# Optimization experiments

Hardware: AMD Instinct MI355X
Metric: run time of the kernel (lower is better)

Reference implementation:

```python
import jax, jax.numpy as jnp
import numpy as np

B, N, Q, D = 1, 6, 10000, 256
HEADS, LEVELS, NPTS, ZANCH = 8, 1, 8, 4  # NPTS = 2*n_points, ZANCH = num_points_in_pillar
HF, WF = 32, 88
HD = D // HEADS


def setup_inputs() -> dict:
    key = jax.random.key(0)
    ks = jax.random.split(key, 18)
    s = 1.0 / np.sqrt(D)
    inp = {
        'queries': jax.random.normal(ks[0], (B, N, Q, D), jnp.float32),
        'pos_emb': jax.random.normal(ks[1], (B, N, Q, D), jnp.float32),
        'lvl_emb': jax.random.normal(ks[2], (LEVELS, D), jnp.float32),
        'cam_emb': jax.random.normal(ks[3], (N, D), jnp.float32),
        'features0': jax.random.normal(ks[4], (B * N, D, HF, WF), jnp.float32),
        'reference_points_3D': jax.random.uniform(ks[5], (B, N, Q, ZANCH, 2), jnp.float32),
        'bev_mask': jax.random.randint(ks[6], (B, N, Q, ZANCH, 2), 0, 2).astype(bool),
        # MSDeformAttn3D params
        'W_value': jax.random.normal(ks[7], (D, D), jnp.float32) * s,
        'b_value': jnp.zeros((D,), jnp.float32),
        'W_off': jax.random.normal(ks[8], (HEADS * LEVELS * NPTS * 2, D), jnp.float32) * 0.01,
        'b_off': jax.random.uniform(ks[9], (HEADS * LEVELS * NPTS * 2,), jnp.float32, -2.0, 2.0),
        'W_attn': jax.random.normal(ks[10], (HEADS * LEVELS * NPTS, D), jnp.float32) * s,
        'b_attn': jnp.zeros((HEADS * LEVELS * NPTS,), jnp.float32),
        'W_inner': jax.random.normal(ks[11], (D, D), jnp.float32) * s,
        'b_inner': jnp.zeros((D,), jnp.float32),
        # SpatialCrossAttention.output_proj
        'W_out': jax.random.normal(ks[12], (D, D), jnp.float32) * s,
        'b_out': jnp.zeros((D,), jnp.float32),
    }
    return inp


def _bilinear(value_t, loc, H, W):
    # value_t: (bn, heads, H*W, hd); loc: (bn, q, heads, pts, 2) normalized to [0,1]
    bn, q, heads, pts, _ = loc.shape
    hd = value_t.shape[-1]
    # grid_sample(2*loc-1, align_corners=False) -> pixel coord = loc*size - 0.5
    x = loc[..., 0] * W - 0.5
    y = loc[..., 1] * H - 0.5
    x0 = jnp.floor(x); y0 = jnp.floor(y)
    dx = x - x0; dy = y - y0
    x0 = x0.astype(jnp.int32); y0 = y0.astype(jnp.int32)
    out = jnp.zeros((bn, heads, q * pts, hd), value_t.dtype)
    corners = ((0, 0, (1 - dx) * (1 - dy)), (1, 0, dx * (1 - dy)),
               (0, 1, (1 - dx) * dy), (1, 1, dx * dy))
    for ox, oy, w in corners:
        xi = x0 + ox; yi = y0 + oy
        valid = (xi >= 0) & (xi < W) & (yi >= 0) & (yi < H)  # zero padding
        wgt = jnp.where(valid, w, 0.0)
        idx = jnp.clip(yi, 0, H - 1) * W + jnp.clip(xi, 0, W - 1)  # (bn,q,heads,pts)
        idx_t = idx.transpose(0, 2, 1, 3).reshape(bn, heads, q * pts)
        g = jnp.take_along_axis(value_t, idx_t[..., None], axis=2)  # (bn,heads,q*pts,hd)
        wgt_t = wgt.transpose(0, 2, 1, 3).reshape(bn, heads, q * pts)
        out = out + g * wgt_t[..., None]
    return out.reshape(bn, heads, q, pts, hd)


def _forward(queries, pos_emb, lvl_emb, cam_emb, features0, reference_points_3D, bev_mask,
             W_value, b_value, W_off, b_off, W_attn, b_attn, W_inner, b_inner, W_out, b_out):
    b, n, q, d = queries.shape
    hf, wf = features0.shape[-2:]
    # flatten features + level/cam embeddings -> (b*n, hw, d)
    feat = features0.reshape(b, n, d, hf * wf)
    feat = feat + lvl_emb[0][None, None, :, None] + cam_emb[None, :, :, None]
    input_flatten = feat.transpose(0, 1, 3, 2).reshape(b * n, hf * wf, d)

    qp = (queries + pos_emb).reshape(b * n, q, d)
    ref = reference_points_3D.reshape(b * n, q, ZANCH, 2)

    # --- MSDeformAttn3D (single level) ---
    value = (input_flatten @ W_value.T + b_value).reshape(b * n, hf * wf, HEADS, HD)
    off = (qp @ W_off.T + b_off).reshape(b * n, q, HEADS, LEVELS, NPTS, 2)
    attw = jax.nn.softmax((qp @ W_attn.T + b_attn).reshape(b * n, q, HEADS, LEVELS * NPTS), axis=-1)
    attw = attw.reshape(b * n, q, HEADS, LEVELS, NPTS)
    normalizer = jnp.array([wf, hf], queries.dtype)  # (W, H)
    pts_per_z = NPTS // ZANCH
    off_z = off.reshape(b * n, q, HEADS, LEVELS, pts_per_z, ZANCH, 2)
    loc = ref[:, :, None, None, None, :, :] + off_z / normalizer
    loc = loc.reshape(b * n, q, HEADS, LEVELS, NPTS, 2)

    value_t = value.transpose(0, 2, 1, 3)  # (bn, heads, hw, hd)
    sampled = _bilinear(value_t, loc[:, :, :, 0], hf, wf)  # (bn,heads,q,pts,hd)
    attw_t = attw[:, :, :, 0].transpose(0, 2, 1, 3)  # (bn,heads,q,pts)
    out = jnp.einsum('bhqp,bhqpc->bqhc', attw_t, sampled).reshape(b * n, q, d)
    out = out @ W_inner.T + b_inner

    # --- scatter back per camera, normalize by hit count ---
    attn = out.reshape(b, n, q, d)
    # indexes come from batch 0's mask (as in the original code)
    hit = (bev_mask[0, :, :, :, 0].astype(jnp.int32).sum(-1) > 0).astype(queries.dtype)  # (n,q)
    slots = (attn * hit[None, :, :, None]).sum(1)  # (b,q,d)
    count = (bev_mask[..., 0].astype(jnp.int32).sum(-1) > 0).astype(queries.dtype).sum(1)
    count = jnp.clip(count, 1.0, None)  # (b,q)
    slots = slots / count[..., None]
    return slots @ W_out.T + b_out


def reference(queries, pos_emb, lvl_emb, cam_emb, features0, reference_points_3D, bev_mask,
              W_value, b_value, W_off, b_off, W_attn, b_attn, W_inner, b_inner, W_out, b_out):
    return _forward(queries, pos_emb, lvl_emb, cam_emb, features0, reference_points_3D, bev_mask,
                    W_value, b_value, W_off, b_off, W_attn, b_attn, W_inner, b_inner, W_out, b_out)
```

## Files before the change

kernel.cpp:

```cpp
#include <hip/hip_runtime.h>
#include <hip/hip_bf16.h>

#define BN     6
#define NQ     10000
#define DIM    256
#define HEADS  8
#define HDD    32
#define HF_    32
#define WF_    88
#define HW_    (HF_*WF_)
#define MTOT   (BN*NQ)

typedef __attribute__((ext_vector_type(8))) unsigned short ushort8_t;
typedef __attribute__((ext_vector_type(8))) short bf16x8;
typedef __attribute__((ext_vector_type(4))) float f32x4;

static __device__ inline unsigned short f2bf(float x) {
    __hip_bfloat16 b = __float2bfloat16(x);
    return *(unsigned short*)&b;
}

__global__ __launch_bounds__(256)
void k_wcvt(const float* __restrict__ Wv, const float* __restrict__ Wo,
            const float* __restrict__ Wa,
            unsigned short* __restrict__ Wv_bf, unsigned short* __restrict__ Woa_bf)
{
    const int i4 = (blockIdx.x*256 + threadIdx.x) * 4;
    if (i4 < 65536) {
        float4 v = *(const float4*)(Wv+i4);
        ushort4 p; p.x=f2bf(v.x);p.y=f2bf(v.y);p.z=f2bf(v.z);p.w=f2bf(v.w);
        *(ushort4*)(Wv_bf+i4) = p;
    }
    if (i4 < 32768) {
        float4 v = *(const float4*)(Wo+i4);
        ushort4 p; p.x=f2bf(v.x);p.y=f2bf(v.y);p.z=f2bf(v.z);p.w=f2bf(v.w);
        *(ushort4*)(Woa_bf+i4) = p;
    }
    if (i4 < 16384) {
        float4 v = *(const float4*)(Wa+i4);
        ushort4 p; p.x=f2bf(v.x);p.y=f2bf(v.y);p.z=f2bf(v.z);p.w=f2bf(v.w);
        *(ushort4*)(Woa_bf+32768+i4) = p;
    }
}

__global__ __launch_bounds__(256)
void k_wcomb(const float* __restrict__ Wz, const float* __restrict__ Wi,
             const float* __restrict__ bi,
             unsigned short* __restrict__ Wzi_bf, float* __restrict__ bzi)
{
    const int j = blockIdx.x;
    const int k = threadIdx.x;
    __shared__ float wzr[DIM];
    wzr[k] = Wz[(size_t)j*DIM + k];
    __syncthreads();
    float s = 0.f;
    for (int t = 0; t < DIM; ++t) s += wzr[t] * Wi[(size_t)t*DIM + k];
    Wzi_bf[(size_t)j*DIM + k] = f2bf(s);
    if (k == 0) {
        float b = 0.f;
        for (int t = 0; t < DIM; ++t) b += wzr[t] * bi[t];
        bzi[j] = b;
    }
}

__global__ __launch_bounds__(256)
void k_ebias(const float* __restrict__ lvl, const float* __restrict__ cam,
             const float* __restrict__ Wv, const float* __restrict__ bv,
             float* __restrict__ ebias)
{
    const int n = blockIdx.x;
    const int j = threadIdx.x;
    __shared__ float e[DIM];
    e[j] = lvl[j] + cam[n*DIM + j];
    __syncthreads();
    const float* w = Wv + (size_t)j*DIM;
    float s = bv[j];
    for (int d = 0; d < DIM; ++d) s += e[d]*w[d];
    ebias[n*DIM + j] = s;
}

__global__ __launch_bounds__(256)
void k_mask(const int* __restrict__ bev, float* __restrict__ hitf,
            float* __restrict__ scale, float* __restrict__ biasf)
{
    const int q = blockIdx.x*256 + threadIdx.x;
    if (q >= NQ) return;
    float cnt = 0.f;
    #pragma unroll
    for (int n = 0; n < BN; ++n) {
        int hit = 0;
        #pragma unroll
        for (int z = 0; z < 4; ++z)
            hit |= (bev[(((size_t)n*NQ + q)*4 + z)*2] != 0);
        hitf[(size_t)n*NQ + q] = (float)hit;
        cnt += (float)hit;
    }
    biasf[q] = (cnt > 0.f) ? 1.f : 0.f;
    scale[q] = 1.f / fmaxf(cnt, 1.f);
}

__global__ __launch_bounds__(256)
void k_feat(const float* __restrict__ feat, unsigned short* __restrict__ featT)
{
    __shared__ float Tf[64][68];
    const int cam = blockIdx.z;
    const int d0 = blockIdx.y * 64;
    const int p0 = blockIdx.x * 64;
    const int tid = threadIdx.x;
    #pragma unroll
    for (int i = 0; i < 4; ++i) {
        const int d = (tid>>4) + i*16;
        const int p4 = (tid&15)*4;
        *(float4*)&Tf[d][p4] = *(const float4*)(feat + ((size_t)cam*DIM + d0 + d)*HW_ + p0 + p4);
    }
    __syncthreads();
    const int p = tid>>2, dq = tid&3;
    unsigned short* ob = featT + ((size_t)cam*HW_ + p0 + p)*DIM + d0;
    #pragma unroll
    for (int i = 0; i < 4; ++i) {
        const int d4 = dq*4 + i*16;
        ushort4 pk;
        pk.x = f2bf(Tf[d4+0][p]); pk.y = f2bf(Tf[d4+1][p]);
        pk.z = f2bf(Tf[d4+2][p]); pk.w = f2bf(Tf[d4+3][p]);
        *(ushort4*)(ob + d4) = pk;
    }
}

__global__ __launch_bounds__(256)
void k_value_mfma(const unsigned short* __restrict__ featT,
                  const unsigned short* __restrict__ Wv_bf,
                  const float* __restrict__ ebias,
                  unsigned short* __restrict__ value_bf)
{
    __shared__ unsigned short Ap[128][72];
    __shared__ unsigned short Bc[64][72];
    const int cam = blockIdx.z;
    const int p0 = blockIdx.x * 128;
    const int c0 = blockIdx.y * 64;
    const int tid = threadIdx.x;
    const int lane = tid & 63, wave = tid >> 6;
    const int quad = lane >> 4, l15 = lane & 15;
    f32x4 acc[2][4] = {};
    const unsigned short* fbase = featT + ((size_t)cam*HW_ + p0)*DIM;

    for (int k0 = 0; k0 < DIM; k0 += 64) {
        #pragma unroll
        for (int i = 0; i < 4; ++i) {
            const int row = (tid>>3) + i*32;
            const int k8 = (tid&7)*8;
            *(ushort8_t*)&Ap[row][k8] = *(const ushort8_t*)(fbase + (size_t)row*DIM + k0 + k8);
        }
        #pragma unroll
        for (int i = 0; i < 2; ++i) {
            const int row = (tid>>3) + i*32;
            const int k8 = (tid&7)*8;
            *(ushort8_t*)&Bc[row][k8] = *(const ushort8_t*)(Wv_bf + (size_t)(c0+row)*DIM + k0 + k8);
        }
        __syncthreads();
        #pragma unroll
        for (int s = 0; s < 2; ++s) {
            const int kf = s*32 + quad*8;
            bf16x8 a[2], b[4];
            #pragma unroll
            for (int mt = 0; mt < 2; ++mt)
                a[mt] = *(const bf16x8*)&Ap[(wave*2+mt)*16 + l15][kf];
            #pragma unroll
            for (int nt = 0; nt < 4; ++nt)
                b[nt] = *(const bf16x8*)&Bc[nt*16 + l15][kf];
            #pragma unroll
            for (int mt = 0; mt < 2; ++mt)
                #pragma unroll
                for (int nt = 0; nt < 4; ++nt)
                    acc[mt][nt] = __builtin_amdgcn_mfma_f32_16x16x32_bf16(a[mt], b[nt], acc[mt][nt], 0,0,0);
        }
        __syncthreads();
    }
    #pragma unroll
    for (int nt = 0; nt < 4; ++nt) {
        const int c = c0 + nt*16 + l15;
        const float eb = ebias[cam*DIM + c];
        const int h = c >> 5, cc = c & 31;
        unsigned short* vb = value_bf + (size_t)(cam*HEADS + h)*HW_*HDD + cc;
        #pragma unroll
        for (int mt = 0; mt < 2; ++mt)
            #pragma unroll
            for (int r = 0; r < 4; ++r) {
                const int p = p0 + (wave*2+mt)*16 + quad*4 + r;
                vb[(size_t)p*HDD] = f2bf(acc[mt][nt][r] + eb);
            }
    }
}

__global__ __launch_bounds__(256, 2)
void k_offattn(const float* __restrict__ Qr, const float* __restrict__ Pe,
               const unsigned short* __restrict__ Woa_bf,
               const float* __restrict__ boff, const float* __restrict__ battn,
               float* __restrict__ off_ws, float* __restrict__ attw_ws)
{
    const int tid = threadIdx.x;
    const int wave = tid >> 6, lane = tid & 63;
    const int quad = lane >> 4, l15 = lane & 15;
    const int m0 = (blockIdx.x*4 + wave) * 16;
    if (m0 >= MTOT) return;

    bf16x8 afr[8];
    {
        const float* qrow = Qr + (size_t)(m0 + l15)*DIM;
        const float* prow = Pe + (size_t)(m0 + l15)*DIM;
        #pragma unroll
        for (int kc = 0; kc < 8; ++kc) {
            const int k = kc*32 + quad*8;
            const float4 x0 = *(const float4*)(qrow + k);
            const float4 x1 = *(const float4*)(qrow + k + 4);
            const float4 y0 = *(const float4*)(prow + k);
            const float4 y1 = *(const float4*)(prow + k + 4);
            ushort8_t u;
            u[0]=f2bf(x0.x+y0.x); u[1]=f2bf(x0.y+y0.y); u[2]=f2bf(x0.z+y0.z); u[3]=f2bf(x0.w+y0.w);
            u[4]=f2bf(x1.x+y1.x); u[5]=f2bf(x1.y+y1.y); u[6]=f2bf(x1.z+y1.z); u[7]=f2bf(x1.w+y1.w);
            afr[kc] = *(bf16x8*)&u;
        }
    }

    f32x4 acc[12] = {};
    const unsigned short* bbase = Woa_bf + (size_t)l15*DIM + quad*8;
    bf16x8 bcur[12], bnxt[12];
    #pragma unroll
    for (int nt = 0; nt < 12; ++nt)
        bcur[nt] = *(const bf16x8*)(bbase + (size_t)nt*16*DIM);
    #pragma unroll
    for (int kc = 0; kc < 8; ++kc) {
        if (kc < 7) {
            #pragma unroll
            for (int nt = 0; nt < 12; ++nt)
                bnxt[nt] = *(const bf16x8*)(bbase + (size_t)nt*16*DIM + (kc+1)*32);
        }
        #pragma unroll
        for (int nt = 0; nt < 12; ++nt)
            acc[nt] = __builtin_amdgcn_mfma_f32_16x16x32_bf16(afr[kc], bcur[nt], acc[nt], 0,0,0);
        #pragma unroll
        for (int nt = 0; nt < 12; ++nt) bcur[nt] = bnxt[nt];
    }

    #pragma unroll
    for (int nt = 0; nt < 12; ++nt) {
        const int col = nt*16 + l15;
        const float bias = (col < 128) ? boff[col] : battn[col-128];
        #pragma unroll
        for (int r = 0; r < 4; ++r) {
            const int m = m0 + quad*4 + r;
            const float v = acc[nt][r] + bias;
            if (col < 128) off_ws [(size_t)m*128 + col]      = v;
            else           attw_ws[(size_t)m*64 + (col-128)] = v;
        }
    }
}

__global__ __launch_bounds__(256)
void k_sample(const unsigned short* __restrict__ value_bf,
              const float* __restrict__ off_ws, const float* __restrict__ attw_ws,
              const float* __restrict__ ref3d, const float* __restrict__ hitf,
              const float* __restrict__ scale, unsigned short* __restrict__ asum_bf)
{
    const int gtid = blockIdx.x*256 + threadIdx.x;
    const int quarter = gtid & 3;
    const int h  = (gtid >> 2) & 7;
    const int q  = gtid >> 5;

    float acc[8];
    #pragma unroll
    for (int c = 0; c < 8; ++c) acc[c] = 0.f;

    #pragma unroll 1
    for (int n = 0; n < BN; ++n) {
        if (hitf[(size_t)n*NQ + q] == 0.f) continue;
        const size_t base = (size_t)n*NQ + q;

        const float4 a0 = *(const float4*)(attw_ws + base*64 + h*8);
        const float4 a1 = *(const float4*)(attw_ws + base*64 + h*8 + 4);
        float lg[8] = {a0.x,a0.y,a0.z,a0.w, a1.x,a1.y,a1.z,a1.w};
        float mx = -1e30f;
        #pragma unroll
        for (int p = 0; p < 8; ++p) mx = fmaxf(mx, lg[p]);
        float ssum = 0.f;
        #pragma unroll
        for (int p = 0; p < 8; ++p) { lg[p] = __expf(lg[p]-mx); ssum += lg[p]; }
        const float inv = 1.f/ssum;

        float off[16];
        #pragma unroll
        for (int i = 0; i < 4; ++i)
            *(float4*)&off[i*4] = *(const float4*)(off_ws + base*128 + h*16 + i*4);
        float ref[8];
        *(float4*)&ref[0] = *(const float4*)(ref3d + base*8);
        *(float4*)&ref[4] = *(const float4*)(ref3d + base*8 + 4);

        const unsigned short* vbase =
            value_bf + (size_t)(n*HEADS + h)*HW_*HDD + quarter*8;

        #pragma unroll
        for (int p = 0; p < 8; ++p) {
            const int z = p & 3;
            const float ax = ref[z*2+0]*WF_ + off[p*2+0] - 0.5f;
            const float ay = ref[z*2+1]*HF_ + off[p*2+1] - 0.5f;
            const float fx = floorf(ax), fy = floorf(ay);
            const float dx = ax-fx, dy = ay-fy;
            const int x0 = (int)fx, y0 = (int)fy;
            const float wp = lg[p]*inv;
            #pragma unroll
            for (int oy = 0; oy < 2; ++oy) {
                const int yi = y0 + oy;
                const float wy = oy ? dy : 1.f-dy;
                #pragma unroll
                for (int ox = 0; ox < 2; ++ox) {
                    const int xi = x0 + ox;
                    const float wx = ox ? dx : 1.f-dx;
                    const bool valid = ((unsigned)xi < WF_) & ((unsigned)yi < HF_);
                    const float cw = valid ? wp*wy*wx : 0.f;
                    const int xc = min(max(xi, 0), WF_-1);
                    const int yc = min(max(yi, 0), HF_-1);
                    const ushort8_t v = *(const ushort8_t*)(vbase + (size_t)(yc*WF_ + xc)*HDD);
                    #pragma unroll
                    for (int c = 0; c < 8; ++c)
                        acc[c] += cw * __uint_as_float(((unsigned)v[c]) << 16);
                }
            }
        }
    }

    const float sc = scale[q];
    ushort8_t o;
    #pragma unroll
    for (int c = 0; c < 8; ++c) o[c] = f2bf(acc[c]*sc);
    *(ushort8_t*)(asum_bf + (size_t)q*DIM + h*HDD + quarter*8) = o;
}

__global__ __launch_bounds__(256)
void k_gemm_mfma(const unsigned short* __restrict__ A_bf,
                 const unsigned short* __restrict__ W_bf,
                 const float* __restrict__ b1, const float* __restrict__ rowscale,
                 const float* __restrict__ b2,
                 float* __restrict__ out_f, int M)
{
    __shared__ unsigned short As[128][72];
    __shared__ unsigned short Bs[64][72];
    const int m0 = blockIdx.x * 128;
    const int j0 = blockIdx.y * 64;
    const int tid = threadIdx.x;
    const int lane = tid & 63, wave = tid >> 6;
    const int quad = lane >> 4, l15 = lane & 15;
    f32x4 acc[2][4] = {};

    for (int k0 = 0; k0 < DIM; k0 += 64) {
        #pragma unroll
        for (int i = 0; i < 4; ++i) {
            const int row = (tid>>3) + i*32;
            const int k8 = (tid&7)*8;
            ushort8_t v = {0,0,0,0,0,0,0,0};
            if (m0 + row < M)
                v = *(const ushort8_t*)(A_bf + (size_t)(m0+row)*DIM + k0 + k8);
            *(ushort8_t*)&As[row][k8] = v;
        }
        #pragma unroll
        for (int i = 0; i < 2; ++i) {
            const int row = (tid>>3) + i*32;
            const int k8 = (tid&7)*8;
            *(ushort8_t*)&Bs[row][k8] = *(const ushort8_t*)(W_bf + (size_t)(j0+row)*DIM + k0 + k8);
        }
        __syncthreads();
        #pragma unroll
        for (int s = 0; s < 2; ++s) {
            const int kf = s*32 + quad*8;
            bf16x8 a[2], b[4];
            #pragma unroll
            for (int mt = 0; mt < 2; ++mt)
                a[mt] = *(const bf16x8*)&As[(wave*2+mt)*16 + l15][kf];
            #pragma unroll
            for (int nt = 0; nt < 4; ++nt)
                b[nt] = *(const bf16x8*)&Bs[nt*16 + l15][kf];
            #pragma unroll
            for (int mt = 0; mt < 2; ++mt)
                #pragma unroll
                for (int nt = 0; nt < 4; ++nt)
                    acc[mt][nt] = __builtin_amdgcn_mfma_f32_16x16x32_bf16(a[mt], b[nt], acc[mt][nt], 0,0,0);
        }
        __syncthreads();
    }
    #pragma unroll
    for (int nt = 0; nt < 4; ++nt) {
        const int j = j0 + nt*16 + l15;
        const float b1j = b1[j], b2j = b2[j];
        #pragma unroll
        for (int mt = 0; mt < 2; ++mt) {
            #pragma unroll
            for (int r = 0; r < 4; ++r) {
                const int m = m0 + (wave*2+mt)*16 + quad*4 + r;
                if (m >= M) continue;
                out_f[(size_t)m*DIM + j] = acc[mt][nt][r] + rowscale[m]*b1j + b2j;
            }
        }
    }
}

extern "C" void kernel_launch(void* const* d_in, const int* in_sizes, int n_in,
                              void* d_out, int out_size, void* d_ws, size_t ws_size,
                              hipStream_t stream)
{
    const float* queries = (const float*)d_in[0];
    const float* pos_emb = (const float*)d_in[1];
    const float* lvl_emb = (const float*)d_in[2];
    const float* cam_emb = (const float*)d_in[3];
    const float* features= (const float*)d_in[4];
    const float* ref3d   = (const float*)d_in[5];
    const int*   bev     = (const int*)d_in[6];
    const float* Wv = (const float*)d_in[7];
    const float* bv = (const float*)d_in[8];
    const float* Wo = (const float*)d_in[9];
    const float* bo = (const float*)d_in[10];
    const float* Wa = (const float*)d_in[11];
    const float* ba = (const float*)d_in[12];
    const float* Wi = (const float*)d_in[13];
    const float* bi = (const float*)d_in[14];
    const float* Wz = (const float*)d_in[15];
    const float* bz = (const float*)d_in[16];
    float* out = (float*)d_out;

    char* ws = (char*)d_ws;
    size_t o = 0;
    auto alloc = [&](size_t bytes) { char* p = ws + o; o += (bytes + 255) & ~size_t(255); return p; };
    unsigned short* value_bf = (unsigned short*)alloc((size_t)BN*HEADS*HW_*HDD*2);
    unsigned short* featT    = (unsigned short*)alloc((size_t)BN*HW_*DIM*2);
    float* off_ws   = (float*)alloc((size_t)MTOT*128*4);
    float* attw_ws  = (float*)alloc((size_t)MTOT*64*4);
    unsigned short* asum_bf  = (unsigned short*)alloc((size_t)NQ*DIM*2);
    unsigned short* Wv_bf  = (unsigned short*)alloc(65536*2);
    unsigned short* Woa_bf = (unsigned short*)alloc(49152*2);
    unsigned short* Wzi_bf = (unsigned short*)alloc(65536*2);
    float* bzi    = (float*)alloc(DIM*4);
    float* hitf   = (float*)alloc((size_t)BN*NQ*4);
    float* scalev = (float*)alloc(NQ*4);
    float* biasf  = (float*)alloc(NQ*4);
    float* ebias  = (float*)alloc(BN*DIM*4);

    k_wcvt  <<<64, 256, 0, stream>>>(Wv, Wo, Wa, Wv_bf, Woa_bf);
    k_wcomb <<<DIM, 256, 0, stream>>>(Wz, Wi, bi, Wzi_bf, bzi);
    k_ebias <<<BN, 256, 0, stream>>>(lvl_emb, cam_emb, Wv, bv, ebias);
    k_mask  <<<(NQ+255)/256, 256, 0, stream>>>(bev, hitf, scalev, biasf);
    k_feat  <<<dim3(HW_/64, DIM/64, BN), 256, 0, stream>>>(features, featT);
    k_value_mfma<<<dim3(HW_/128, DIM/64, BN), 256, 0, stream>>>(featT, Wv_bf, ebias, value_bf);
    k_offattn<<<(MTOT/16 + 3)/4, 256, 0, stream>>>(queries, pos_emb, Woa_bf, bo, ba, off_ws, attw_ws);
    k_sample <<<NQ*32/256, 256, 0, stream>>>(value_bf, off_ws, attw_ws, ref3d, hitf, scalev, asum_bf);
    k_gemm_mfma<<<dim3((NQ+127)/128, DIM/64), 256, 0, stream>>>(asum_bf, Wzi_bf, bzi, biasf, bz, out, NQ);
}
```

Measured before the change: 372.2 us.

## Stage offset/attention weights in LDS and use persistent blocks over two tiles

The offset/attention projection kernel now stages the 192x128 bf16 weight half-slab in shared memory per K-phase and reads B fragments from LDS. Each 512-thread block handles two 16-row tiles per wave across 256 blocks. Before, every wave streamed the whole weight matrix from global or L2. This cuts repeated weight traffic but adds syncs, LDS bank pressure and doubled accumulator registers, and it caps the grid at 256 blocks.

```diff
diff --git a/kernel.cpp b/kernel.cpp
--- a/kernel.cpp
+++ b/kernel.cpp
@@ -10,6 +10,7 @@
 #define WF_    88
 #define HW_    (HF_*WF_)
 #define MTOT   (BN*NQ)
+#define NTILES (MTOT/16)
 
 typedef __attribute__((ext_vector_type(8))) unsigned short ushort8_t;
 typedef __attribute__((ext_vector_type(8))) short bf16x8;
@@ -191,66 +192,83 @@
     }
 }
 
-__global__ __launch_bounds__(256, 2)
+__global__ __launch_bounds__(512)
 void k_offattn(const float* __restrict__ Qr, const float* __restrict__ Pe,
                const unsigned short* __restrict__ Woa_bf,
                const float* __restrict__ boff, const float* __restrict__ battn,
                float* __restrict__ off_ws, float* __restrict__ attw_ws)
 {
-    const int tid = threadIdx.x;
+    __shared__ unsigned short Bw[192][132];
+    const int tid  = threadIdx.x;
     const int wave = tid >> 6, lane = tid & 63;
     const int quad = lane >> 4, l15 = lane & 15;
-    const int m0 = (blockIdx.x*4 + wave) * 16;
-    if (m0 >= MTOT) return;
-
-    bf16x8 afr[8];
-    {
-        const float* qrow = Qr + (size_t)(m0 + l15)*DIM;
-        const float* prow = Pe + (size_t)(m0 + l15)*DIM;
-        #pragma unroll
-        for (int kc = 0; kc < 8; ++kc) {
-            const int k = kc*32 + quad*8;
-            const float4 x0 = *(const float4*)(qrow + k);
-            const float4 x1 = *(const float4*)(qrow + k + 4);
-            const float4 y0 = *(const float4*)(prow + k);
-            const float4 y1 = *(const float4*)(prow + k + 4);
-            ushort8_t u;
-            u[0]=f2bf(x0.x+y0.x); u[1]=f2bf(x0.y+y0.y); u[2]=f2bf(x0.z+y0.z); u[3]=f2bf(x0.w+y0.w);
-            u[4]=f2bf(x1.x+y1.x); u[5]=f2bf(x1.y+y1.y); u[6]=f2bf(x1.z+y1.z); u[7]=f2bf(x1.w+y1.w);
-            afr[kc] = *(bf16x8*)&u;
-        }
-    }
-
-    f32x4 acc[12] = {};
-    const unsigned short* bbase = Woa_bf + (size_t)l15*DIM + quad*8;
-    bf16x8 bcur[12], bnxt[12];
-    #pragma unroll
-    for (int nt = 0; nt < 12; ++nt)
-        bcur[nt] = *(const bf16x8*)(bbase + (size_t)nt*16*DIM);
-    #pragma unroll
-    for (int kc = 0; kc < 8; ++kc) {
-        if (kc < 7) {
-            #pragma unroll
-            for (int nt = 0; nt < 12; ++nt)
-                bnxt[nt] = *(const bf16x8*)(bbase + (size_t)nt*16*DIM + (kc+1)*32);
-        }
-        #pragma unroll
-        for (int nt = 0; nt < 12; ++nt)
-            acc[nt] = __builtin_amdgcn_mfma_f32_16x16x32_bf16(afr[kc], bcur[nt], acc[nt], 0,0,0);
-        #pragma unroll
-        for (int nt = 0; nt < 12; ++nt) bcur[nt] = bnxt[nt];
-    }
-
-    #pragma unroll
-    for (int nt = 0; nt < 12; ++nt) {
-        const int col = nt*16 + l15;
-        const float bias = (col < 128) ? boff[col] : battn[col-128];
-        #pragma unroll
-        for (int r = 0; r < 4; ++r) {
-            const int m = m0 + quad*4 + r;
-            const float v = acc[nt][r] + bias;
-            if (col < 128) off_ws [(size_t)m*128 + col]      = v;
-            else           attw_ws[(size_t)m*64 + (col-128)] = v;
+    const int t0 = blockIdx.x*8 + wave;
+    const int t1 = t0 + 2048;
+
+    f32x4 acc[2][12] = {};
+
+    #pragma unroll
+    for (int phase = 0; phase < 2; ++phase) {
+        if (phase) __syncthreads();
+        #pragma unroll
+        for (int j = 0; j < 6; ++j) {
+            const int u   = tid + j*512;
+            const int row = u >> 4;
+            const int c8  = (u & 15) * 8;
+            *(ushort8_t*)&Bw[row][c8] =
+                *(const ushort8_t*)(Woa_bf + (size_t)row*DIM + phase*128 + c8);
+        }
+        __syncthreads();
+
+        #pragma unroll
+        for (int ti = 0; ti < 2; ++ti) {
+            const int tile = ti ? t1 : t0;
+            if (tile >= NTILES) break;
+            const int m0 = tile * 16;
+
+            bf16x8 afr[4];
+            const float* qrow = Qr + (size_t)(m0 + l15)*DIM + phase*128;
+            const float* prow = Pe + (size_t)(m0 + l15)*DIM + phase*128;
+            #pragma unroll
+            for (int kc = 0; kc < 4; ++kc) {
+                const int k = kc*32 + quad*8;
+                const float4 x0 = *(const float4*)(qrow + k);
+                const float4 x1 = *(const float4*)(qrow + k + 4);
+                const float4 y0 = *(const float4*)(prow + k);
+                const float4 y1 = *(const float4*)(prow + k + 4);
+                ushort8_t u;
+                u[0]=f2bf(x0.x+y0.x); u[1]=f2bf(x0.y+y0.y); u[2]=f2bf(x0.z+y0.z); u[3]=f2bf(x0.w+y0.w);
+                u[4]=f2bf(x1.x+y1.x); u[5]=f2bf(x1.y+y1.y); u[6]=f2bf(x1.z+y1.z); u[7]=f2bf(x1.w+y1.w);
+                afr[kc] = *(bf16x8*)&u;
+            }
+            #pragma unroll
+            for (int kc = 0; kc < 4; ++kc) {
+                const int kf = kc*32 + quad*8;
+                #pragma unroll
+                for (int nt = 0; nt < 12; ++nt) {
+                    const bf16x8 b = *(const bf16x8*)&Bw[nt*16 + l15][kf];
+                    acc[ti][nt] = __builtin_amdgcn_mfma_f32_16x16x32_bf16(afr[kc], b, acc[ti][nt], 0,0,0);
+                }
+            }
+        }
+    }
+
+    #pragma unroll
+    for (int ti = 0; ti < 2; ++ti) {
+        const int tile = ti ? t1 : t0;
+        if (tile >= NTILES) break;
+        const int m0 = tile * 16;
+        #pragma unroll
+        for (int nt = 0; nt < 12; ++nt) {
+            const int col = nt*16 + l15;
+            const float bias = (col < 128) ? boff[col] : battn[col-128];
+            #pragma unroll
+            for (int r = 0; r < 4; ++r) {
+                const int m = m0 + quad*4 + r;
+                const float v = acc[ti][nt][r] + bias;
+                if (col < 128) off_ws [(size_t)m*128 + col]      = v;
+                else           attw_ws[(size_t)m*64 + (col-128)] = v;
+            }
         }
     }
 }
@@ -447,7 +465,7 @@
     k_mask  <<<(NQ+255)/256, 256, 0, stream>>>(bev, hitf, scalev, biasf);
     k_feat  <<<dim3(HW_/64, DIM/64, BN), 256, 0, stream>>>(features, featT);
     k_value_mfma<<<dim3(HW_/128, DIM/64, BN), 256, 0, stream>>>(featT, Wv_bf, ebias, value_bf);
-    k_offattn<<<(MTOT/16 + 3)/4, 256, 0, stream>>>(queries, pos_emb, Woa_bf, bo, ba, off_ws, attw_ws);
+    k_offattn<<<256, 512, 0, stream>>>(queries, pos_emb, Woa_bf, bo, ba, off_ws, attw_ws);
     k_sample <<<NQ*32/256, 256, 0, stream>>>(value_bf, off_ws, attw_ws, ref3d, hitf, scalev, asum_bf);
     k_gemm_mfma<<<dim3((NQ+127)/128, DIM/64), 256, 0, stream>>>(asum_bf, Wzi_bf, bzi, biasf, bz, out, NQ);
 }
```

Measured after the change: 361.2 us. 1.03x faster.
